# Kernel tuning notes

Hardware: AMD Instinct MI355X
Metric: run time of the kernel (lower is better)

Reference implementation:

```python
import jax, jax.numpy as jnp
import numpy as np

B, V = 256, 2048
PD, MD, H = 1024, 512, 512

def setup_inputs() -> dict:
    key = jax.random.key(0)
    k1, k2, k3, k4, k5 = jax.random.split(key, 5)
    patient_emb = jax.random.normal(k1, (B, PD), dtype=jnp.float32)
    atc4_emb = jax.random.normal(k2, (V, MD), dtype=jnp.float32)
    # Linear(PD+MD -> H): weight (H, PD+MD), bias (H,)
    W1 = jax.random.normal(k3, (H, PD + MD), dtype=jnp.float32) * 0.02
    b1 = jnp.zeros((H,), dtype=jnp.float32)
    # Linear(H -> 1): weight (1, H) -> store as (H,), bias scalar
    w2 = jax.random.normal(k4, (H,), dtype=jnp.float32) * 0.05
    b2 = jnp.zeros((), dtype=jnp.float32)
    return {"patient_emb": patient_emb, "atc4_emb": atc4_emb,
            "W1": W1, "b1": b1, "w2": w2, "b2": b2}

def reference(patient_emb, atc4_emb, W1, b1, w2, b2):
    # Algebraically equivalent to cat([patient, mol]) @ W1.T:
    # split W1 into patient and mol blocks, matmul each, broadcast-add.
    W1p = W1[:, :PD]   # (H, PD)
    W1m = W1[:, PD:]   # (H, MD)
    hp = jnp.einsum('bp,hp->bh', patient_emb, W1p)   # (B, H)
    hm = jnp.einsum('vm,hm->vh', atc4_emb, W1m)      # (V, H)
    h = jnp.tanh(hp[:, None, :] + hm[None, :, :] + b1)  # (B, V, H)
    scores = jnp.einsum('bvh,h->bv', h, w2) + b2     # (B, V)
    return scores
```

## Files before the change

### kernel.cpp

```cpp
#include <hip/hip_runtime.h>
#include <hip/hip_bf16.h>
#include <math.h>

typedef __attribute__((ext_vector_type(8))) short short8;
typedef __attribute__((ext_vector_type(4))) short short4v;
typedef __attribute__((ext_vector_type(4))) float float4v;
typedef __attribute__((ext_vector_type(2))) float float2v;

__device__ __forceinline__ short f2bf(float f) {
    union { float f; unsigned u; } x; x.f = f;
    unsigned r = (x.u + 0x7FFFu + ((x.u >> 16) & 1u)) >> 16;
    return (short)r;
}

__global__ __launch_bounds__(256) void gemm_exp(
    const float* __restrict__ patient, const float* __restrict__ atc4,
    const float* __restrict__ W1, const float* __restrict__ b1,
    float* __restrict__ EA, float* __restrict__ EM)
{
    const float* A; const float* W; const float* bias; float* T;
    int lda, K, M;
    if (blockIdx.z == 0) {
        if (blockIdx.x >= 4) return;
        A = patient; lda = 1024; K = 1024; M = 256; bias = b1; T = EA; W = W1;
    } else {
        A = atc4;    lda = 512;  K = 512;  M = 2048; bias = nullptr; T = EM; W = W1 + 1024;
    }
    const int ldw = 1536;

    __shared__ short As[64][72];
    __shared__ short Bs[64][72];
    const int t = threadIdx.x;
    const int m0 = blockIdx.x * 64;
    const int n0 = blockIdx.y * 64;
    const int wave = t >> 6;
    const int lane = t & 63;
    const int wm = (wave & 1) * 32;
    const int wn = (wave >> 1) * 32;
    const int lrow = lane & 15;
    const int quad = lane >> 4;

    float4v acc[2][2];
    #pragma unroll
    for (int i = 0; i < 2; i++)
        #pragma unroll
        for (int j = 0; j < 2; j++)
            acc[i][j] = (float4v){0.f, 0.f, 0.f, 0.f};

    const int sr = t >> 2;
    const int sc = (t & 3) * 16;

    for (int k0 = 0; k0 < K; k0 += 64) {
        const float* ap = A + (size_t)(m0 + sr) * lda + (k0 + sc);
        const float* wp = W + (size_t)(n0 + sr) * ldw + (k0 + sc);
        #pragma unroll
        for (int ii = 0; ii < 4; ii++) {
            float4v av = *(const float4v*)(ap + ii * 4);
            float4v wv = *(const float4v*)(wp + ii * 4);
            short4v a4 = { f2bf(av.x), f2bf(av.y), f2bf(av.z), f2bf(av.w) };
            short4v w4 = { f2bf(wv.x), f2bf(wv.y), f2bf(wv.z), f2bf(wv.w) };
            *(short4v*)&As[sr][sc + ii * 4] = a4;
            *(short4v*)&Bs[sr][sc + ii * 4] = w4;
        }
        __syncthreads();
        #pragma unroll
        for (int kk = 0; kk < 64; kk += 32) {
            short8 af[2], bfr[2];
            #pragma unroll
            for (int i = 0; i < 2; i++)
                af[i] = *(const short8*)&As[wm + i * 16 + lrow][kk + quad * 8];
            #pragma unroll
            for (int j = 0; j < 2; j++)
                bfr[j] = *(const short8*)&Bs[wn + j * 16 + lrow][kk + quad * 8];
            #pragma unroll
            for (int i = 0; i < 2; i++)
                #pragma unroll
                for (int j = 0; j < 2; j++)
                    acc[i][j] = __builtin_amdgcn_mfma_f32_16x16x32_bf16(
                        af[i], bfr[j], acc[i][j], 0, 0, 0);
        }
        __syncthreads();
    }

    #pragma unroll
    for (int i = 0; i < 2; i++) {
        #pragma unroll
        for (int j = 0; j < 2; j++) {
            const int n  = n0 + wn + j * 16 + lrow;
            const int mb = m0 + wm + i * 16 + quad * 4;
            const float bn = bias ? bias[n] : 0.0f;
            float4v ev;
            #pragma unroll
            for (int r = 0; r < 4; r++)
                ev[r] = __expf(2.0f * (acc[i][j][r] + bn));
            *(float4v*)&T[(size_t)n * M + mb] = ev;
        }
    }
}

__global__ __launch_bounds__(256, 8) void pair_kernel(
    const float* __restrict__ EA, const float* __restrict__ EM,
    const float* __restrict__ w2, float* __restrict__ partial)
{
    __shared__ float sEA[32][36];
    __shared__ float sEM[32][68];
    __shared__ float2v sC[32];
    const int t  = threadIdx.x;
    const int v0 = blockIdx.x * 64;
    const int b0 = blockIdx.y * 32;
    const int h0 = blockIdx.z * 64;
    const int tx = t & 15;
    const int ty = t >> 4;

    if (t < 32) {
        float2v c = { -2.0f * w2[h0 + 2 * t], -2.0f * w2[h0 + 2 * t + 1] };
        sC[t] = c;
    }

    float4v acc[2];
    acc[0] = (float4v){0.f, 0.f, 0.f, 0.f};
    acc[1] = (float4v){0.f, 0.f, 0.f, 0.f};
    const float4v one4 = {1.f, 1.f, 1.f, 1.f};

    const int rS = t >> 3;
    const int cA = (t & 7) * 4;
    const int cM = (t & 7) * 8;

    float4v pA, pM0, pM1;
    {
        pA  = *(const float4v*)(EA + (size_t)(h0 + rS) * 256 + b0 + cA);
        const float* pm = EM + (size_t)(h0 + rS) * 2048 + v0 + cM;
        pM0 = *(const float4v*)pm;  pM1 = *(const float4v*)(pm + 4);
    }
    *(float4v*)&sEA[rS][cA] = pA;
    *(float4v*)&sEM[rS][cM] = pM0;  *(float4v*)&sEM[rS][cM + 4] = pM1;
    __syncthreads();
    {
        pA  = *(const float4v*)(EA + (size_t)(h0 + 32 + rS) * 256 + b0 + cA);
        const float* pm = EM + (size_t)(h0 + 32 + rS) * 2048 + v0 + cM;
        pM0 = *(const float4v*)pm;  pM1 = *(const float4v*)(pm + 4);
    }

    #pragma unroll
    for (int half = 0; half < 2; half++) {
        #pragma unroll 2
        for (int hp = 0; hp < 16; hp++) {
            const int ha = 2 * hp, hb = 2 * hp + 1;
            const float4v em0 = *(const float4v*)&sEM[ha][tx * 4];
            const float4v em1 = *(const float4v*)&sEM[hb][tx * 4];
            const float2v c = sC[half * 16 + hp];
            const float4v c0 = { c.x, c.x, c.x, c.x };
            const float4v c1 = { c.y, c.y, c.y, c.y };
            #pragma unroll
            for (int i = 0; i < 2; i++) {
                const float ea0 = sEA[ha][ty * 2 + i];
                const float ea1 = sEA[hb][ty * 2 + i];
                const float4v ea0v = { ea0, ea0, ea0, ea0 };
                const float4v ea1v = { ea1, ea1, ea1, ea1 };
                float4v d0  = __builtin_elementwise_fma(em0, ea0v, one4);
                float4v d1  = __builtin_elementwise_fma(em1, ea1v, one4);
                float4v den = d0 * d1;
                float4v num = __builtin_elementwise_fma(d1, c0, d0 * c1);
                float4v r = { __builtin_amdgcn_rcpf(den.x),
                              __builtin_amdgcn_rcpf(den.y),
                              __builtin_amdgcn_rcpf(den.z),
                              __builtin_amdgcn_rcpf(den.w) };
                acc[i] = __builtin_elementwise_fma(num, r, acc[i]);
            }
        }
        if (half == 0) {
            __syncthreads();
            *(float4v*)&sEA[rS][cA] = pA;
            *(float4v*)&sEM[rS][cM] = pM0;  *(float4v*)&sEM[rS][cM + 4] = pM1;
            __syncthreads();
        }
    }

    float2v w2p = sC[0];
    for (int k = 1; k < 32; k++) w2p += sC[k];
    const float w2s = -0.5f * (w2p.x + w2p.y);

    const size_t pb = (size_t)blockIdx.z * (256 * 2048);
    #pragma unroll
    for (int i = 0; i < 2; i++) {
        float4v o = acc[i] + w2s;
        *(float4v*)&partial[pb + (size_t)(b0 + ty * 2 + i) * 2048 + v0 + tx * 4] = o;
    }
}

__global__ __launch_bounds__(256) void reduce_kernel(
    const float* __restrict__ partial, const float* __restrict__ b2,
    float* __restrict__ out)
{
    const int i = (blockIdx.x * 256 + threadIdx.x) * 4;
    const float bb = b2[0];
    float4v s = *(const float4v*)&partial[i];
    #pragma unroll
    for (int z = 1; z < 8; z++)
        s += *(const float4v*)&partial[(size_t)z * 524288 + i];
    float4v o = s + bb;
    *(float4v*)&out[i] = o;
}

extern "C" void kernel_launch(void* const* d_in, const int* in_sizes, int n_in,
                              void* d_out, int out_size, void* d_ws, size_t ws_size,
                              hipStream_t stream)
{
    const float* patient = (const float*)d_in[0];
    const float* atc4    = (const float*)d_in[1];
    const float* W1      = (const float*)d_in[2];
    const float* b1      = (const float*)d_in[3];
    const float* w2      = (const float*)d_in[4];
    const float* b2      = (const float*)d_in[5];
    float* out = (float*)d_out;
    float* ws  = (float*)d_ws;

    float* EA      = ws;
    float* EM      = ws + 131072;
    float* partial = ws + 1179648;

    gemm_exp<<<dim3(32, 8, 2), 256, 0, stream>>>(patient, atc4, W1, b1, EA, EM);
    pair_kernel<<<dim3(32, 8, 8), 256, 0, stream>>>(EA, EM, w2, partial);
    reduce_kernel<<<512, 256, 0, stream>>>(partial, b2, out);
}
```

Before: 121.8 us.

## Combine four tanh terms per reciprocal and fuse split-H reduction via atomic counters

The pair kernel now merges four h-terms per reciprocal instead of two, cutting the rcp count in half at the cost of extra multiplies and larger intermediate products that could overflow for large exp values. The separate reduce kernel is removed. The last of the eight h-slice blocks for each output tile, found with an atomic counter (reset inside gemm_exp), sums the partials and writes the output, saving one kernel launch. It also switches the bf16 conversion to packed intrinsics, loads sEA as float2, and lowers the occupancy hint in launch_bounds from 8 to 4.

New measurement: 308.0 us. 153% more time.

```diff
diff --git a/kernel.cpp b/kernel.cpp
--- a/kernel.cpp
+++ b/kernel.cpp
@@ -7,21 +7,26 @@
 typedef __attribute__((ext_vector_type(4))) float float4v;
 typedef __attribute__((ext_vector_type(2))) float float2v;
 
-__device__ __forceinline__ short f2bf(float f) {
-    union { float f; unsigned u; } x; x.f = f;
-    unsigned r = (x.u + 0x7FFFu + ((x.u >> 16) & 1u)) >> 16;
-    return (short)r;
+__device__ __forceinline__ int2 cvt2bf16x4(float4v v) {
+    union { __hip_bfloat162 h2; int i; } u0, u1;
+    u0.h2 = __float22bfloat162_rn(make_float2(v.x, v.y));
+    u1.h2 = __float22bfloat162_rn(make_float2(v.z, v.w));
+    return make_int2(u0.i, u1.i);
 }
 
 __global__ __launch_bounds__(256) void gemm_exp(
     const float* __restrict__ patient, const float* __restrict__ atc4,
     const float* __restrict__ W1, const float* __restrict__ b1,
-    float* __restrict__ EA, float* __restrict__ EM)
+    float* __restrict__ EA, float* __restrict__ EM, unsigned* __restrict__ counters)
 {
     const float* A; const float* W; const float* bias; float* T;
     int lda, K, M;
     if (blockIdx.z == 0) {
-        if (blockIdx.x >= 4) return;
+        if (blockIdx.x >= 4) {
+            if (blockIdx.x == 4 && blockIdx.y == 0)
+                counters[threadIdx.x] = 0u;
+            return;
+        }
         A = patient; lda = 1024; K = 1024; M = 256; bias = b1; T = EA; W = W1;
     } else {
         A = atc4;    lda = 512;  K = 512;  M = 2048; bias = nullptr; T = EM; W = W1 + 1024;
@@ -57,10 +62,8 @@
         for (int ii = 0; ii < 4; ii++) {
             float4v av = *(const float4v*)(ap + ii * 4);
             float4v wv = *(const float4v*)(wp + ii * 4);
-            short4v a4 = { f2bf(av.x), f2bf(av.y), f2bf(av.z), f2bf(av.w) };
-            short4v w4 = { f2bf(wv.x), f2bf(wv.y), f2bf(wv.z), f2bf(wv.w) };
-            *(short4v*)&As[sr][sc + ii * 4] = a4;
-            *(short4v*)&Bs[sr][sc + ii * 4] = w4;
+            *(int2*)&As[sr][sc + ii * 4] = cvt2bf16x4(av);
+            *(int2*)&Bs[sr][sc + ii * 4] = cvt2bf16x4(wv);
         }
         __syncthreads();
         #pragma unroll
@@ -98,13 +101,16 @@
     }
 }
 
-__global__ __launch_bounds__(256, 8) void pair_kernel(
+__global__ __launch_bounds__(256, 4) void pair_kernel(
     const float* __restrict__ EA, const float* __restrict__ EM,
-    const float* __restrict__ w2, float* __restrict__ partial)
+    const float* __restrict__ w2, const float* __restrict__ b2,
+    float* __restrict__ partial, unsigned* __restrict__ counters,
+    float* __restrict__ out)
 {
     __shared__ float sEA[32][36];
     __shared__ float sEM[32][68];
-    __shared__ float2v sC[32];
+    __shared__ float4v sC4[16];
+    __shared__ unsigned sFlag;
     const int t  = threadIdx.x;
     const int v0 = blockIdx.x * 64;
     const int b0 = blockIdx.y * 32;
@@ -112,9 +118,9 @@
     const int tx = t & 15;
     const int ty = t >> 4;
 
-    if (t < 32) {
-        float2v c = { -2.0f * w2[h0 + 2 * t], -2.0f * w2[h0 + 2 * t + 1] };
-        sC[t] = c;
+    if (t < 16) {
+        float4v wv = *(const float4v*)(w2 + h0 + 4 * t);
+        sC4[t] = -2.0f * wv;
     }
 
     float4v acc[2];
@@ -144,23 +150,37 @@
     #pragma unroll
     for (int half = 0; half < 2; half++) {
         #pragma unroll 2
-        for (int hp = 0; hp < 16; hp++) {
-            const int ha = 2 * hp, hb = 2 * hp + 1;
-            const float4v em0 = *(const float4v*)&sEM[ha][tx * 4];
-            const float4v em1 = *(const float4v*)&sEM[hb][tx * 4];
-            const float2v c = sC[half * 16 + hp];
+        for (int q = 0; q < 8; q++) {
+            const int hq = 4 * q;
+            const float4v em0 = *(const float4v*)&sEM[hq    ][tx * 4];
+            const float4v em1 = *(const float4v*)&sEM[hq + 1][tx * 4];
+            const float4v em2 = *(const float4v*)&sEM[hq + 2][tx * 4];
+            const float4v em3 = *(const float4v*)&sEM[hq + 3][tx * 4];
+            const float2v ea0 = *(const float2v*)&sEA[hq    ][ty * 2];
+            const float2v ea1 = *(const float2v*)&sEA[hq + 1][ty * 2];
+            const float2v ea2 = *(const float2v*)&sEA[hq + 2][ty * 2];
+            const float2v ea3 = *(const float2v*)&sEA[hq + 3][ty * 2];
+            const float4v c = sC4[half * 8 + q];
             const float4v c0 = { c.x, c.x, c.x, c.x };
             const float4v c1 = { c.y, c.y, c.y, c.y };
+            const float4v c2 = { c.z, c.z, c.z, c.z };
+            const float4v c3 = { c.w, c.w, c.w, c.w };
             #pragma unroll
             for (int i = 0; i < 2; i++) {
-                const float ea0 = sEA[ha][ty * 2 + i];
-                const float ea1 = sEA[hb][ty * 2 + i];
-                const float4v ea0v = { ea0, ea0, ea0, ea0 };
-                const float4v ea1v = { ea1, ea1, ea1, ea1 };
-                float4v d0  = __builtin_elementwise_fma(em0, ea0v, one4);
-                float4v d1  = __builtin_elementwise_fma(em1, ea1v, one4);
-                float4v den = d0 * d1;
-                float4v num = __builtin_elementwise_fma(d1, c0, d0 * c1);
+                const float4v a0 = { ea0[i], ea0[i], ea0[i], ea0[i] };
+                const float4v a1 = { ea1[i], ea1[i], ea1[i], ea1[i] };
+                const float4v a2 = { ea2[i], ea2[i], ea2[i], ea2[i] };
+                const float4v a3 = { ea3[i], ea3[i], ea3[i], ea3[i] };
+                float4v d0 = __builtin_elementwise_fma(em0, a0, one4);
+                float4v d1 = __builtin_elementwise_fma(em1, a1, one4);
+                float4v d2 = __builtin_elementwise_fma(em2, a2, one4);
+                float4v d3 = __builtin_elementwise_fma(em3, a3, one4);
+                float4v e01 = d0 * d1;
+                float4v e23 = d2 * d3;
+                float4v n01 = __builtin_elementwise_fma(d1, c0, d0 * c1);
+                float4v n23 = __builtin_elementwise_fma(d3, c2, d2 * c3);
+                float4v num = __builtin_elementwise_fma(n01, e23, n23 * e01);
+                float4v den = e01 * e23;
                 float4v r = { __builtin_amdgcn_rcpf(den.x),
                               __builtin_amdgcn_rcpf(den.y),
                               __builtin_amdgcn_rcpf(den.z),
@@ -176,9 +196,9 @@
         }
     }
 
-    float2v w2p = sC[0];
-    for (int k = 1; k < 32; k++) w2p += sC[k];
-    const float w2s = -0.5f * (w2p.x + w2p.y);
+    float4v w2q = sC4[0];
+    for (int k = 1; k < 16; k++) w2q += sC4[k];
+    const float w2s = -0.5f * (w2q.x + w2q.y + w2q.z + w2q.w);
 
     const size_t pb = (size_t)blockIdx.z * (256 * 2048);
     #pragma unroll
@@ -186,20 +206,29 @@
         float4v o = acc[i] + w2s;
         *(float4v*)&partial[pb + (size_t)(b0 + ty * 2 + i) * 2048 + v0 + tx * 4] = o;
     }
-}
-
-__global__ __launch_bounds__(256) void reduce_kernel(
-    const float* __restrict__ partial, const float* __restrict__ b2,
-    float* __restrict__ out)
-{
-    const int i = (blockIdx.x * 256 + threadIdx.x) * 4;
-    const float bb = b2[0];
-    float4v s = *(const float4v*)&partial[i];
-    #pragma unroll
-    for (int z = 1; z < 8; z++)
-        s += *(const float4v*)&partial[(size_t)z * 524288 + i];
-    float4v o = s + bb;
-    *(float4v*)&out[i] = o;
+
+    __threadfence();
+    if (t == 0) {
+        const unsigned old = atomicAdd(&counters[blockIdx.y * 32 + blockIdx.x], 1u);
+        sFlag = (old == 7u) ? 1u : 0u;
+    }
+    __syncthreads();
+    if (sFlag) {
+        __threadfence();
+        const float bb = b2[0];
+        #pragma unroll
+        for (int e = 0; e < 2; e++) {
+            const int f  = t * 2 + e;
+            const int br = f >> 4;
+            const int vc = (f & 15) * 4;
+            const size_t off = (size_t)(b0 + br) * 2048 + v0 + vc;
+            float4v s = { bb, bb, bb, bb };
+            #pragma unroll
+            for (int z = 0; z < 8; z++)
+                s += *(const float4v*)&partial[(size_t)z * 524288 + off];
+            *(float4v*)&out[off] = s;
+        }
+    }
 }
 
 extern "C" void kernel_launch(void* const* d_in, const int* in_sizes, int n_in,
@@ -215,11 +244,13 @@
     float* out = (float*)d_out;
     float* ws  = (float*)d_ws;
 
-    float* EA      = ws;
-    float* EM      = ws + 131072;
-    float* partial = ws + 1179648;
-
-    gemm_exp<<<dim3(32, 8, 2), 256, 0, stream>>>(patient, atc4, W1, b1, EA, EM);
-    pair_kernel<<<dim3(32, 8, 8), 256, 0, stream>>>(EA, EM, w2, partial);
-    reduce_kernel<<<512, 256, 0, stream>>>(partial, b2, out);
-}
+    float* EA         = ws;
+    float* EM         = ws + 131072;
+    float* partial    = ws + 1179648;
+    unsigned* counters = (unsigned*)(ws + 1179648 + 4194304);
+
+    gemm_exp<<<dim3(32, 8, 2), 256, 0, stream>>>(patient, atc4, W1, b1, EA, EM,
+                                                 counters);
+    pair_kernel<<<dim3(32, 8, 8), 256, 0, stream>>>(EA, EM, w2, b2, partial,
+                                                    counters, out);
+}
```
